# Performance work log

Measured on AMD Instinct MI355X. Metric: run time of the kernel, lower is better.

## Reference

```python
import jax, jax.numpy as jnp
import numpy as np

NU0, NI0 = 20000, 15000
NU1, NI1 = 4000, 3000
N0, N1 = NU0 + NI0, NU1 + NI1
E0, E1 = 1_000_000, 200_000
D, L = 64, 3
EPS = 1e-12  # F.normalize eps


def setup_inputs() -> dict:
    key = jax.random.key(0)
    ks = jax.random.split(key, 20)
    s = 0.1
    inp = {
        'ue0': jax.random.normal(ks[0], (NU0, D), jnp.float32) * s,
        'ie0': jax.random.normal(ks[1], (NI0, D), jnp.float32) * s,
        'gcW0': jax.random.normal(ks[2], (L, D, D), jnp.float32) * s,
        'gcb0': jax.random.normal(ks[3], (L, D), jnp.float32) * s,
        'biW0': jax.random.normal(ks[4], (L, D, D), jnp.float32) * s,
        'bib0': jax.random.normal(ks[5], (L, D), jnp.float32) * s,
        'ue1': jax.random.normal(ks[6], (NU1, D), jnp.float32) * s,
        'ie1': jax.random.normal(ks[7], (NI1, D), jnp.float32) * s,
        'gcW1': jax.random.normal(ks[8], (L, D, D), jnp.float32) * s,
        'gcb1': jax.random.normal(ks[9], (L, D), jnp.float32) * s,
        'biW1': jax.random.normal(ks[10], (L, D, D), jnp.float32) * s,
        'bib1': jax.random.normal(ks[11], (L, D), jnp.float32) * s,
        'mapu': jax.random.normal(ks[12], (NU0, NU1), jnp.float32) * 0.01,
        'mapi': jax.random.normal(ks[13], (NI0, NI1), jnp.float32) * 0.01,
        'vals0': jax.random.uniform(ks[14], (E0,), jnp.float32) * 0.01,
        'vals1': jax.random.uniform(ks[15], (E1,), jnp.float32) * 0.01,
        'rows0': jax.random.randint(ks[16], (E0,), 0, N0, jnp.int32),
        'cols0': jax.random.randint(ks[17], (E0,), 0, N0, jnp.int32),
        'rows1': jax.random.randint(ks[18], (E1,), 0, N1, jnp.int32),
        'cols1': jax.random.randint(ks[19], (E1,), 0, N1, jnp.int32),
    }
    return inp


def _ngcf(ue, ie, gcW, gcb, biW, bib, rows, cols, vals, n_users, n_nodes):
    # ego: [N, D]; dropout is identity (eval / p=0)
    ego = jnp.concatenate([ue, ie], axis=0)
    outs = [ego]
    for i in range(L):
        # sparse adj @ ego: gather cols, scale by edge value, scatter-add to rows
        side = jax.ops.segment_sum(vals[:, None] * ego[cols], rows, num_segments=n_nodes)
        sum_e = jax.nn.leaky_relu(side @ gcW[i] + gcb[i], negative_slope=0.01)
        bi_e = jax.nn.leaky_relu((ego * side) @ biW[i] + bib[i], negative_slope=0.01)
        ego = sum_e + bi_e
        norm = ego / jnp.maximum(jnp.linalg.norm(ego, axis=1, keepdims=True), EPS)
        outs.append(norm)
    all_e = jnp.concatenate(outs, axis=1)  # [N, D*(L+1)]
    return all_e[:n_users], all_e[n_users:]


def reference(ue0, ie0, gcW0, gcb0, biW0, bib0,
              ue1, ie1, gcW1, gcb1, biW1, bib1,
              mapu, mapi, vals0, vals1,
              rows0, cols0, rows1, cols1):
    ug0, ig0 = _ngcf(ue0, ie0, gcW0, gcb0, biW0, bib0, rows0, cols0, vals0, NU0, N0)
    ug1, ig1 = _ngcf(ue1, ie1, gcW1, gcb1, biW1, bib1, rows1, cols1, vals1, NU1, N1)
    user_embd = ug0 + mapu @ ug1   # [NU0, 256]
    item_embd = ig0 + mapi @ ig1   # [NI0, 256]
    return (user_embd, item_embd)
```

## Files before the change

### kernel.cpp

```cpp
#include <hip/hip_runtime.h>

#define NU0 20000
#define NI0 15000
#define NN0 35000
#define NU1 4000
#define NI1 3000
#define NN1 7000
#define EE0 1000000
#define EE1 200000
#define KP_I 3008

typedef _Float16 f16;
typedef _Float16 f16x4 __attribute__((ext_vector_type(4)));
typedef _Float16 f16x8 __attribute__((ext_vector_type(8)));
typedef float f32x4 __attribute__((ext_vector_type(4)));

__global__ void k_init_ego(const float* __restrict__ ue, const float* __restrict__ ie,
                           int nu, int n, float* __restrict__ ego, float* __restrict__ alle) {
    int tid = blockIdx.x * blockDim.x + threadIdx.x;
    if (tid >= n * 64) return;
    int row = tid >> 6, c = tid & 63;
    float v = (row < nu) ? ue[tid] : ie[tid - nu * 64];
    ego[tid] = v;
    alle[(size_t)row * 256 + c] = v;
}

__global__ void k_hist(const int* __restrict__ rows, int e, int* __restrict__ cnt) {
    int tid = blockIdx.x * blockDim.x + threadIdx.x;
    if (tid < e) atomicAdd(&cnt[rows[tid]], 1);
}

__global__ __launch_bounds__(1024) void k_scan(const int* __restrict__ cnt, int n,
                                               int* __restrict__ rowptr, int* __restrict__ fill) {
    __shared__ int sm[1024];
    __shared__ int carry;
    int tid = threadIdx.x;
    if (tid == 0) { carry = 0; rowptr[0] = 0; }
    __syncthreads();
    for (int base = 0; base < n; base += 1024) {
        int i = base + tid;
        int v = (i < n) ? cnt[i] : 0;
        sm[tid] = v;
        __syncthreads();
        for (int off = 1; off < 1024; off <<= 1) {
            int t = (tid >= off) ? sm[tid - off] : 0;
            __syncthreads();
            sm[tid] += t;
            __syncthreads();
        }
        int incl = sm[tid];
        int total = sm[1023];
        int c = carry;
        if (i < n) { rowptr[i + 1] = c + incl; fill[i] = c + incl - v; }
        __syncthreads();
        if (tid == 0) carry += total;
        __syncthreads();
    }
}

__global__ void k_scatter(const int* __restrict__ rows, const int* __restrict__ cols,
                          const float* __restrict__ vals, int e, int* __restrict__ fill,
                          int* __restrict__ colss, float* __restrict__ valss) {
    int tid = blockIdx.x * blockDim.x + threadIdx.x;
    if (tid < e) {
        int r = rows[tid];
        int pos = atomicAdd(&fill[r], 1);
        colss[pos] = cols[tid];
        valss[pos] = vals[tid];
    }
}

__global__ void k_spmm(const int* __restrict__ rowptr, const int* __restrict__ colss,
                       const float* __restrict__ valss, const float* __restrict__ ego,
                       float* __restrict__ side, int nrows) {
    int gw = (blockIdx.x * blockDim.x + threadIdx.x) >> 6;
    int lane = threadIdx.x & 63;
    if (gw >= nrows) return;
    int s = rowptr[gw];
    int e = rowptr[gw + 1];
    s = __builtin_amdgcn_readfirstlane(s);
    e = __builtin_amdgcn_readfirstlane(e);
    float acc = 0.f;
    for (int i = s; i < e; ++i) {
        int c = colss[i];
        float v = valss[i];
        acc += v * ego[(size_t)c * 64 + lane];
    }
    side[(size_t)gw * 64 + lane] = acc;
}

#define DPAD 72
__global__ __launch_bounds__(256) void k_dense(
    const float* __restrict__ side, float* __restrict__ ego,
    const float* __restrict__ Wg, const float* __restrict__ bg,
    const float* __restrict__ Wb, const float* __restrict__ bb,
    float* __restrict__ alle, int col_off, int nrows) {
    __shared__ f16 sS[64 * DPAD];
    __shared__ f16 sM[64 * DPAD];
    __shared__ f16 sWg[64 * DPAD];
    __shared__ f16 sWb[64 * DPAD];
    int tid = threadIdx.x;
    int m0 = blockIdx.x * 64;
#pragma unroll
    for (int j = 0; j < 16; j++) {
        int idx = j * 256 + tid;
        int k = idx >> 6, nn = idx & 63;
        sWg[nn * DPAD + k] = (f16)Wg[idx];
        sWb[nn * DPAD + k] = (f16)Wb[idx];
    }
    {
        int row = tid >> 2;
        int seg = (tid & 3) * 16;
        bool rok = (m0 + row) < nrows;
        const float4* sp = (const float4*)(side + (size_t)(m0 + row) * 64 + seg);
        const float4* ep = (const float4*)(ego + (size_t)(m0 + row) * 64 + seg);
#pragma unroll
        for (int j = 0; j < 4; j++) {
            float4 sv = rok ? sp[j] : make_float4(0.f, 0.f, 0.f, 0.f);
            float4 ev = rok ? ep[j] : make_float4(0.f, 0.f, 0.f, 0.f);
            f16x4 a, m;
            a[0] = (f16)sv.x; a[1] = (f16)sv.y; a[2] = (f16)sv.z; a[3] = (f16)sv.w;
            m[0] = (f16)(sv.x * ev.x); m[1] = (f16)(sv.y * ev.y);
            m[2] = (f16)(sv.z * ev.z); m[3] = (f16)(sv.w * ev.w);
            int kk = seg + j * 4;
            *(f16x4*)&sS[row * DPAD + kk] = a;
            *(f16x4*)&sM[row * DPAD + kk] = m;
        }
    }
    __syncthreads();
    int lane = tid & 63, wv = tid >> 6;
    int lr = lane & 15, quad = lane >> 4;
    int wm = wv * 16;
    f32x4 zero = {0.f, 0.f, 0.f, 0.f};
    f32x4 accA[4], accB[4];
#pragma unroll
    for (int j = 0; j < 4; j++) { accA[j] = zero; accB[j] = zero; }
#pragma unroll
    for (int k0 = 0; k0 < 64; k0 += 32) {
        f16x8 af = *(f16x8*)&sS[(wm + lr) * DPAD + k0 + quad * 8];
        f16x8 mf = *(f16x8*)&sM[(wm + lr) * DPAD + k0 + quad * 8];
#pragma unroll
        for (int j = 0; j < 4; j++) {
            f16x8 bgf = *(f16x8*)&sWg[(j * 16 + lr) * DPAD + k0 + quad * 8];
            f16x8 bbf = *(f16x8*)&sWb[(j * 16 + lr) * DPAD + k0 + quad * 8];
            accA[j] = __builtin_amdgcn_mfma_f32_16x16x32_f16(af, bgf, accA[j], 0, 0, 0);
            accB[j] = __builtin_amdgcn_mfma_f32_16x16x32_f16(mf, bbf, accB[j], 0, 0, 0);
        }
    }
    float e[4][4];
    float sq[4] = {0.f, 0.f, 0.f, 0.f};
#pragma unroll
    for (int j = 0; j < 4; j++) {
        int col = j * 16 + lr;
        float bgv = bg[col], bbv = bb[col];
#pragma unroll
        for (int r = 0; r < 4; r++) {
            float a = accA[j][r] + bgv; a = (a > 0.f) ? a : 0.01f * a;
            float b = accB[j][r] + bbv; b = (b > 0.f) ? b : 0.01f * b;
            float ev = a + b;
            e[j][r] = ev;
            sq[r] += ev * ev;
        }
    }
#pragma unroll
    for (int msk = 1; msk < 16; msk <<= 1) {
#pragma unroll
        for (int r = 0; r < 4; r++) sq[r] += __shfl_xor(sq[r], msk, 64);
    }
#pragma unroll
    for (int r = 0; r < 4; r++) {
        int gr = m0 + wm + quad * 4 + r;
        if (gr < nrows) {
            float inv = 1.0f / fmaxf(sqrtf(sq[r]), 1e-12f);
#pragma unroll
            for (int j = 0; j < 4; j++) {
                int col = j * 16 + lr;
                ego[(size_t)gr * 64 + col] = e[j][r];
                alle[(size_t)gr * 256 + col_off + col] = e[j][r] * inv;
            }
        }
    }
}

__global__ void k_transpose(const float* __restrict__ src, f16* __restrict__ dst, int K, int Kp) {
    int k = blockIdx.x * blockDim.x + threadIdx.x;
    int nIdx = blockIdx.y;
    if (k < Kp)
        dst[(size_t)nIdx * Kp + k] = (k < K) ? (f16)src[(size_t)k * 256 + nIdx] : (f16)0.f;
}

#define GPAD 40
__global__ __launch_bounds__(256) void k_gemm(
    const float* __restrict__ A, const f16* __restrict__ Bt,
    const float* __restrict__ C0, float* __restrict__ outp,
    int M, int K, int Kp) {
    __shared__ f16 sA[128 * GPAD];
    __shared__ f16 sB[128 * GPAD];
    int tid = threadIdx.x;
    int bm = blockIdx.x >> 1, bn = blockIdx.x & 1;
    int m0 = bm * 128, n0 = bn * 128;
    int lane = tid & 63, wv = tid >> 6;
    int lr = lane & 15, quad = lane >> 4;
    int wm = (wv >> 1) * 64, wn = (wv & 1) * 64;
    int srow = tid >> 1;
    int skh = (tid & 1) * 16;
    bool arow_ok = (m0 + srow) < M;
    const float* aptr = A + (size_t)(m0 + srow) * K + skh;
    const f16* bptr = Bt + (size_t)(n0 + srow) * Kp + skh;
    f32x4 zero = {0.f, 0.f, 0.f, 0.f};
    f32x4 acc[4][4];
#pragma unroll
    for (int i = 0; i < 4; i++)
#pragma unroll
        for (int j = 0; j < 4; j++) acc[i][j] = zero;
    for (int k0 = 0; k0 < Kp; k0 += 32) {
#pragma unroll
        for (int j = 0; j < 4; j++) {
            int kk = k0 + skh + j * 4;
            float4 v = make_float4(0.f, 0.f, 0.f, 0.f);
            if (arow_ok && kk < K) v = *(const float4*)(aptr + k0 + j * 4);
            f16x4 h;
            h[0] = (f16)v.x; h[1] = (f16)v.y; h[2] = (f16)v.z; h[3] = (f16)v.w;
            *(f16x4*)&sA[srow * GPAD + skh + j * 4] = h;
        }
        *(f16x8*)&sB[srow * GPAD + skh] = *(const f16x8*)(bptr + k0);
        *(f16x8*)&sB[srow * GPAD + skh + 8] = *(const f16x8*)(bptr + k0 + 8);
        __syncthreads();
        f16x8 af[4], bf[4];
#pragma unroll
        for (int i = 0; i < 4; i++) af[i] = *(f16x8*)&sA[(wm + i * 16 + lr) * GPAD + quad * 8];
#pragma unroll
        for (int j = 0; j < 4; j++) bf[j] = *(f16x8*)&sB[(wn + j * 16 + lr) * GPAD + quad * 8];
#pragma unroll
        for (int i = 0; i < 4; i++)
#pragma unroll
            for (int j = 0; j < 4; j++)
                acc[i][j] = __builtin_amdgcn_mfma_f32_16x16x32_f16(af[i], bf[j], acc[i][j], 0, 0, 0);
        __syncthreads();
    }
#pragma unroll
    for (int i = 0; i < 4; i++) {
#pragma unroll
        for (int r = 0; r < 4; r++) {
            int gr = m0 + wm + i * 16 + quad * 4 + r;
            if (gr < M) {
#pragma unroll
                for (int j = 0; j < 4; j++) {
                    int gc = n0 + wn + j * 16 + lr;
                    size_t off = (size_t)gr * 256 + gc;
                    outp[off] = acc[i][j][r] + C0[off];
                }
            }
        }
    }
}

extern "C" void kernel_launch(void* const* d_in, const int* in_sizes, int n_in,
                              void* d_out, int out_size, void* d_ws, size_t ws_size,
                              hipStream_t stream) {
    (void)in_sizes; (void)n_in; (void)out_size; (void)ws_size;
    const float* ue0  = (const float*)d_in[0];
    const float* ie0  = (const float*)d_in[1];
    const float* gcW0 = (const float*)d_in[2];
    const float* gcb0 = (const float*)d_in[3];
    const float* biW0 = (const float*)d_in[4];
    const float* bib0 = (const float*)d_in[5];
    const float* ue1  = (const float*)d_in[6];
    const float* ie1  = (const float*)d_in[7];
    const float* gcW1 = (const float*)d_in[8];
    const float* gcb1 = (const float*)d_in[9];
    const float* biW1 = (const float*)d_in[10];
    const float* bib1 = (const float*)d_in[11];
    const float* mapu = (const float*)d_in[12];
    const float* mapi = (const float*)d_in[13];
    const float* vals0 = (const float*)d_in[14];
    const float* vals1 = (const float*)d_in[15];
    const int* rows0 = (const int*)d_in[16];
    const int* cols0 = (const int*)d_in[17];
    const int* rows1 = (const int*)d_in[18];
    const int* cols1 = (const int*)d_in[19];
    float* out = (float*)d_out;

    char* p = (char*)d_ws;
    auto alloc = [&](size_t b) { char* r = p; p += (b + 255) & ~(size_t)255; return r; };
    float* ego0  = (float*)alloc((size_t)NN0 * 64 * 4);
    float* side0 = (float*)alloc((size_t)NN0 * 64 * 4);
    float* alle0 = (float*)alloc((size_t)NN0 * 256 * 4);
    float* ego1  = (float*)alloc((size_t)NN1 * 64 * 4);
    float* side1 = (float*)alloc((size_t)NN1 * 64 * 4);
    float* alle1 = (float*)alloc((size_t)NN1 * 256 * 4);
    int* cnt0    = (int*)alloc((size_t)NN0 * 4);
    int* ptr0    = (int*)alloc((size_t)(NN0 + 1) * 4);
    int* fill0   = (int*)alloc((size_t)NN0 * 4);
    int* colss0  = (int*)alloc((size_t)EE0 * 4);
    float* valss0 = (float*)alloc((size_t)EE0 * 4);
    int* cnt1    = (int*)alloc((size_t)NN1 * 4);
    int* ptr1    = (int*)alloc((size_t)(NN1 + 1) * 4);
    int* fill1   = (int*)alloc((size_t)NN1 * 4);
    int* colss1  = (int*)alloc((size_t)EE1 * 4);
    float* valss1 = (float*)alloc((size_t)EE1 * 4);
    f16* btu = (f16*)alloc((size_t)256 * 4000 * 2);
    f16* bti = (f16*)alloc((size_t)256 * KP_I * 2);

    hipMemsetAsync(cnt0, 0, (size_t)NN0 * 4, stream);
    hipMemsetAsync(cnt1, 0, (size_t)NN1 * 4, stream);

    k_init_ego<<<(NN0 * 64 + 255) / 256, 256, 0, stream>>>(ue0, ie0, NU0, NN0, ego0, alle0);
    k_init_ego<<<(NN1 * 64 + 255) / 256, 256, 0, stream>>>(ue1, ie1, NU1, NN1, ego1, alle1);

    k_hist<<<(EE0 + 255) / 256, 256, 0, stream>>>(rows0, EE0, cnt0);
    k_hist<<<(EE1 + 255) / 256, 256, 0, stream>>>(rows1, EE1, cnt1);
    k_scan<<<1, 1024, 0, stream>>>(cnt0, NN0, ptr0, fill0);
    k_scan<<<1, 1024, 0, stream>>>(cnt1, NN1, ptr1, fill1);
    k_scatter<<<(EE0 + 255) / 256, 256, 0, stream>>>(rows0, cols0, vals0, EE0, fill0, colss0, valss0);
    k_scatter<<<(EE1 + 255) / 256, 256, 0, stream>>>(rows1, cols1, vals1, EE1, fill1, colss1, valss1);

    for (int l = 0; l < 3; l++) {
        k_spmm<<<(NN0 * 64 + 255) / 256, 256, 0, stream>>>(ptr0, colss0, valss0, ego0, side0, NN0);
        k_dense<<<(NN0 + 63) / 64, 256, 0, stream>>>(side0, ego0, gcW0 + l * 4096, gcb0 + l * 64,
                                                     biW0 + l * 4096, bib0 + l * 64, alle0, (l + 1) * 64, NN0);
        k_spmm<<<(NN1 * 64 + 255) / 256, 256, 0, stream>>>(ptr1, colss1, valss1, ego1, side1, NN1);
        k_dense<<<(NN1 + 63) / 64, 256, 0, stream>>>(side1, ego1, gcW1 + l * 4096, gcb1 + l * 64,
                                                     biW1 + l * 4096, bib1 + l * 64, alle1, (l + 1) * 64, NN1);
    }

    dim3 tgu((4000 + 255) / 256, 256);
    k_transpose<<<tgu, 256, 0, stream>>>(alle1, btu, 4000, 4000);
    dim3 tgi((KP_I + 255) / 256, 256);
    k_transpose<<<tgi, 256, 0, stream>>>(alle1 + (size_t)4000 * 256, bti, 3000, KP_I);

    k_gemm<<<((NU0 + 127) / 128) * 2, 256, 0, stream>>>(mapu, btu, alle0, out, NU0, 4000, 4000);
    k_gemm<<<((NI0 + 127) / 128) * 2, 256, 0, stream>>>(mapi, bti, alle0 + (size_t)NU0 * 256,
                                                        out + (size_t)NU0 * 256, NI0, 3000, KP_I);
}
```

Baseline: 1.422 ms.

## Split-K GEMM with atomic accumulation into output, warp-shuffle scan, unrolled SpMM

The final mapping GEMMs are split along K into four chunks per tile, and each chunk atomically adds its partial sum into the output. The output buffer now doubles as the graph-embedding buffer, so the base term is already in place and the separate C0 read is gone. This is meant to fix low occupancy, since only about 314 blocks were launched before. Separately, the row-pointer scan uses wave shuffles instead of a shared-memory Hillis-Steele loop, and the SpMM gather is unrolled by four to expose more memory-level parallelism. The atomics add global traffic and make the floating-point summation order nondeterministic.

```diff
diff --git a/kernel.cpp b/kernel.cpp
--- a/kernel.cpp
+++ b/kernel.cpp
@@ -9,6 +9,7 @@
 #define EE0 1000000
 #define EE1 200000
 #define KP_I 3008
+#define NSPLIT 4
 
 typedef _Float16 f16;
 typedef _Float16 f16x4 __attribute__((ext_vector_type(4)));
@@ -32,28 +33,39 @@
 
 __global__ __launch_bounds__(1024) void k_scan(const int* __restrict__ cnt, int n,
                                                int* __restrict__ rowptr, int* __restrict__ fill) {
-    __shared__ int sm[1024];
-    __shared__ int carry;
+    __shared__ int wsum[16];
+    __shared__ int carry_s;
     int tid = threadIdx.x;
-    if (tid == 0) { carry = 0; rowptr[0] = 0; }
+    int lane = tid & 63, wv = tid >> 6;
+    if (tid == 0) { carry_s = 0; rowptr[0] = 0; }
     __syncthreads();
     for (int base = 0; base < n; base += 1024) {
         int i = base + tid;
         int v = (i < n) ? cnt[i] : 0;
-        sm[tid] = v;
-        __syncthreads();
-        for (int off = 1; off < 1024; off <<= 1) {
-            int t = (tid >= off) ? sm[tid - off] : 0;
-            __syncthreads();
-            sm[tid] += t;
-            __syncthreads();
-        }
-        int incl = sm[tid];
-        int total = sm[1023];
-        int c = carry;
+        int x = v;
+#pragma unroll
+        for (int off = 1; off < 64; off <<= 1) {
+            int t = __shfl_up(x, off, 64);
+            if (lane >= off) x += t;
+        }
+        if (lane == 63) wsum[wv] = x;
+        __syncthreads();
+        if (wv == 0 && lane < 16) {
+            int y = wsum[lane];
+#pragma unroll
+            for (int off = 1; off < 16; off <<= 1) {
+                int t = __shfl_up(y, off, 16);
+                if (lane >= off) y += t;
+            }
+            wsum[lane] = y;
+        }
+        __syncthreads();
+        int blocksum = wsum[15];
+        int incl = x + (wv ? wsum[wv - 1] : 0);
+        int c = carry_s;
         if (i < n) { rowptr[i + 1] = c + incl; fill[i] = c + incl - v; }
         __syncthreads();
-        if (tid == 0) carry += total;
+        if (tid == 0) carry_s += blocksum;
         __syncthreads();
     }
 }
@@ -81,10 +93,18 @@
     s = __builtin_amdgcn_readfirstlane(s);
     e = __builtin_amdgcn_readfirstlane(e);
     float acc = 0.f;
-    for (int i = s; i < e; ++i) {
-        int c = colss[i];
-        float v = valss[i];
-        acc += v * ego[(size_t)c * 64 + lane];
+    int i = s;
+    for (; i + 3 < e; i += 4) {
+        int c0 = colss[i], c1 = colss[i + 1], c2 = colss[i + 2], c3 = colss[i + 3];
+        float v0 = valss[i], v1 = valss[i + 1], v2 = valss[i + 2], v3 = valss[i + 3];
+        float g0 = ego[(size_t)c0 * 64 + lane];
+        float g1 = ego[(size_t)c1 * 64 + lane];
+        float g2 = ego[(size_t)c2 * 64 + lane];
+        float g3 = ego[(size_t)c3 * 64 + lane];
+        acc += v0 * g0 + v1 * g1 + v2 * g2 + v3 * g3;
+    }
+    for (; i < e; ++i) {
+        acc += valss[i] * ego[(size_t)colss[i] * 64 + lane];
     }
     side[(size_t)gw * 64 + lane] = acc;
 }
@@ -192,13 +212,17 @@
 #define GPAD 40
 __global__ __launch_bounds__(256) void k_gemm(
     const float* __restrict__ A, const f16* __restrict__ Bt,
-    const float* __restrict__ C0, float* __restrict__ outp,
-    int M, int K, int Kp) {
+    float* __restrict__ outp, int M, int K, int Kp) {
     __shared__ f16 sA[128 * GPAD];
     __shared__ f16 sB[128 * GPAD];
     int tid = threadIdx.x;
-    int bm = blockIdx.x >> 1, bn = blockIdx.x & 1;
+    int split = blockIdx.x % NSPLIT;
+    int t = blockIdx.x / NSPLIT;
+    int bm = t >> 1, bn = t & 1;
     int m0 = bm * 128, n0 = bn * 128;
+    int chunk = ((Kp / 32 + NSPLIT - 1) / NSPLIT) * 32;
+    int kbeg = split * chunk;
+    int kend = min(Kp, kbeg + chunk);
     int lane = tid & 63, wv = tid >> 6;
     int lr = lane & 15, quad = lane >> 4;
     int wm = (wv >> 1) * 64, wn = (wv & 1) * 64;
@@ -213,7 +237,7 @@
     for (int i = 0; i < 4; i++)
 #pragma unroll
         for (int j = 0; j < 4; j++) acc[i][j] = zero;
-    for (int k0 = 0; k0 < Kp; k0 += 32) {
+    for (int k0 = kbeg; k0 < kend; k0 += 32) {
 #pragma unroll
         for (int j = 0; j < 4; j++) {
             int kk = k0 + skh + j * 4;
@@ -248,7 +272,7 @@
                 for (int j = 0; j < 4; j++) {
                     int gc = n0 + wn + j * 16 + lr;
                     size_t off = (size_t)gr * 256 + gc;
-                    outp[off] = acc[i][j][r] + C0[off];
+                    atomicAdd(&outp[off], acc[i][j][r]);
                 }
             }
         }
@@ -285,7 +309,7 @@
     auto alloc = [&](size_t b) { char* r = p; p += (b + 255) & ~(size_t)255; return r; };
     float* ego0  = (float*)alloc((size_t)NN0 * 64 * 4);
     float* side0 = (float*)alloc((size_t)NN0 * 64 * 4);
-    float* alle0 = (float*)alloc((size_t)NN0 * 256 * 4);
+    float* alle0 = out;
     float* ego1  = (float*)alloc((size_t)NN1 * 64 * 4);
     float* side1 = (float*)alloc((size_t)NN1 * 64 * 4);
     float* alle1 = (float*)alloc((size_t)NN1 * 256 * 4);
@@ -329,7 +353,7 @@
     dim3 tgi((KP_I + 255) / 256, 256);
     k_transpose<<<tgi, 256, 0, stream>>>(alle1 + (size_t)4000 * 256, bti, 3000, KP_I);
 
-    k_gemm<<<((NU0 + 127) / 128) * 2, 256, 0, stream>>>(mapu, btu, alle0, out, NU0, 4000, 4000);
-    k_gemm<<<((NI0 + 127) / 128) * 2, 256, 0, stream>>>(mapi, bti, alle0 + (size_t)NU0 * 256,
+    k_gemm<<<((NU0 + 127) / 128) * 2 * NSPLIT, 256, 0, stream>>>(mapu, btu, out, NU0, 4000, 4000);
+    k_gemm<<<((NI0 + 127) / 128) * 2 * NSPLIT, 256, 0, stream>>>(mapi, bti,
                                                         out + (size_t)NU0 * 256, NI0, 3000, KP_I);
 }
```

Measured after the change: 1.204 ms. -15.3%, faster.
